# Optimization experiments

Measured on AMD Instinct MI355X. Metric: run time of the kernel, lower is better.

The kernel has to match this reference:

```python
import jax, jax.numpy as jnp
import numpy as np

B, N, F_IN, D, DEPTH = 16, 1024, 80, 64, 4
BN_EPS = 1e-5

def setup_inputs() -> dict:
    key = jax.random.key(0)
    ks = jax.random.split(key, 24)
    def xavier(k, shape, gain):
        fan_in, fan_out = shape[0], shape[-1]
        a = gain * np.sqrt(6.0 / (fan_in + fan_out))
        return jax.random.uniform(k, shape, jnp.float32, -a, a)
    g_relu = float(np.sqrt(2.0))
    g_lrelu = float(np.sqrt(2.0 / (1 + 0.01 ** 2)))
    adj = jax.random.randint(ks[0], (B, N, N), 0, 2, jnp.int32)
    X = jax.random.normal(ks[1], (B, N, F_IN), jnp.float32)
    root_list = jax.random.randint(ks[2], (B, DEPTH, N), 0, 2).astype(jnp.float32)
    W0 = xavier(ks[3], (F_IN, D), g_lrelu)
    Wl = jnp.stack([xavier(ks[4 + i], (D, D), g_relu) for i in range(3)])
    a1l = jnp.stack([xavier(ks[7 + i], (D, 1), g_relu)[:, 0] for i in range(3)])
    a2l = jnp.stack([xavier(ks[10 + i], (D, 1), g_relu)[:, 0] for i in range(3)])
    P = xavier(ks[13], (1, D), g_relu)
    def linear(k, din, dout):
        a = 1.0 / np.sqrt(din)
        k1, k2 = jax.random.split(k)
        return (jax.random.uniform(k1, (din, dout), jnp.float32, -a, a),
                jax.random.uniform(k2, (dout,), jnp.float32, -a, a))
    pW1, pb1 = linear(ks[14], D, 128)
    pW2, pb2 = linear(ks[15], 128, 64)
    pW3, pb3 = linear(ks[16], 64, 2)
    bn = lambda n: (jnp.ones((n,), jnp.float32), jnp.zeros((n,), jnp.float32),
                    jnp.zeros((n,), jnp.float32), jnp.ones((n,), jnp.float32))
    g1, be1, m1, v1 = bn(128)
    g2, be2, m2, v2 = bn(64)
    return dict(adj=adj, X=X, root_list=root_list, W0=W0, Wl=Wl, a1l=a1l, a2l=a2l, P=P,
                pW1=pW1, pb1=pb1, g1=g1, be1=be1, m1=m1, v1=v1,
                pW2=pW2, pb2=pb2, g2=g2, be2=be2, m2=m2, v2=v2,
                pW3=pW3, pb3=pb3)

def reference(adj, X, root_list, W0, Wl, a1l, a2l, P,
              pW1, pb1, g1, be1, m1, v1, pW2, pb2, g2, be2, m2, v2, pW3, pb3):
    relu = jax.nn.relu
    # initial feature change
    h = relu(jnp.einsum('bnf,fd->bnd', X, W0))
    adj_pos = adj > 0
    for i in range(DEPTH - 1):
        root = root_list[:, DEPTH - 1 - i, :]            # [B,N]
        h0 = h
        hW = relu(jnp.einsum('bnd,de->bne', h, Wl[i]))    # [B,N,D]
        t1 = jnp.einsum('bnd,d->bn', hW, a1l[i])
        t2 = jnp.einsum('bnd,d->bn', hW, a2l[i])
        e = relu(t1[:, :, None] + t2[:, None, :])         # [B,N,N]
        # NOTE: original uses -9e15 * zeros_like(adj) == 0 as the masked fill value
        e = jnp.where(adj_pos, e, jnp.zeros((), e.dtype))
        att = jax.nn.softmax(e, axis=-1)
        emb = jnp.einsum('bnm,bmd->bnd', att, hW)
        # assign = root^T @ ones broadcasts root over d
        h = jnp.where(root[:, :, None] > 0, emb, h0)
    # readout attention over root nodes (last root used: depth index 1)
    root = root_list[:, 1, :]
    e = relu(jnp.einsum('d,bnd->bn', P[0], h))
    e = jnp.where(root > 0, e, jnp.float32(-9e15))
    att = jax.nn.softmax(e, axis=-1)
    out = jnp.einsum('bn,bnd->bd', att, h)                # [B,D]
    # prediction head (eval mode: BN uses running stats, dropout off)
    def bn_apply(x, g, be, m, v):
        return (x - m) * jax.lax.rsqrt(v + BN_EPS) * g + be
    x = relu(bn_apply(out @ pW1 + pb1, g1, be1, m1, v1))
    x = relu(bn_apply(x @ pW2 + pb2, g2, be2, m2, v2))
    logits = relu(x @ pW3 + pb3)
    return jax.nn.softmax(logits, axis=-1)
```

## Files before the change

kernel.cpp:

```cpp
#include <hip/hip_runtime.h>
#include <hip/hip_bf16.h>
#include <math.h>

#define B 16
#define N 1024
#define F_IN 80
#define D 64
#define DEPTH 4
#define BN_EPS 1e-5f

typedef __attribute__((ext_vector_type(8))) short  short8v;
typedef __attribute__((ext_vector_type(4))) float  float4v;

union AFrag { unsigned int u[4]; short8v s; };

__device__ __forceinline__ unsigned short f2bf_rne(float x) {
    unsigned int u = __float_as_uint(x);
    unsigned int r = u + 0x7FFFu + ((u >> 16) & 1u);
    return (unsigned short)(r >> 16);
}
__device__ __forceinline__ float bf2f(unsigned short b) {
    return __uint_as_float(((unsigned int)b) << 16);
}

__global__ __launch_bounds__(256) void k_pack(const int* __restrict__ adj,
                                              unsigned short* __restrict__ packS) {
    int gid = blockIdx.x * 256 + threadIdx.x;
    const int4* ap = (const int4*)adj + (size_t)gid * 4;
    unsigned int m = 0;
#pragma unroll
    for (int i = 0; i < 4; ++i) {
        int4 v = ap[i];
        m |= (unsigned int)(v.x > 0) << (i * 4 + 0);
        m |= (unsigned int)(v.y > 0) << (i * 4 + 1);
        m |= (unsigned int)(v.z > 0) << (i * 4 + 2);
        m |= (unsigned int)(v.w > 0) << (i * 4 + 3);
    }
    packS[gid] = (unsigned short)m;
}

__global__ __launch_bounds__(256) void k_h0(const float* __restrict__ X,
                                            const float* __restrict__ W0,
                                            float* __restrict__ h) {
    int b = blockIdx.x >> 6, n0 = (blockIdx.x & 63) << 4;
    int t = threadIdx.x;
    __shared__ float w0s[F_IN * D];
    __shared__ float xs[16 * F_IN];
    for (int j = t; j < F_IN * D; j += 256) w0s[j] = W0[j];
    const float* xp = X + ((size_t)(b * N + n0)) * F_IN;
    for (int j = t; j < 16 * F_IN; j += 256) xs[j] = xp[j];
    __syncthreads();
    int d = t & 63, wid = t >> 6;
    float acc[4] = {0.f, 0.f, 0.f, 0.f};
    for (int f = 0; f < F_IN; ++f) {
        float wv = w0s[f * D + d];
#pragma unroll
        for (int j = 0; j < 4; ++j) acc[j] += xs[(wid * 4 + j) * F_IN + f] * wv;
    }
    float* hp = h + ((size_t)(b * N + n0 + wid * 4)) * D + d;
#pragma unroll
    for (int j = 0; j < 4; ++j) hp[(size_t)j * D] = fmaxf(acc[j], 0.f);
}

__global__ __launch_bounds__(256) void k_hw(const float* __restrict__ h,
                                            const float* __restrict__ Wl,
                                            const float* __restrict__ a1,
                                            const float* __restrict__ a2,
                                            unsigned short* __restrict__ hWhi,
                                            unsigned short* __restrict__ hWlo,
                                            float* __restrict__ t1,
                                            float* __restrict__ t2) {
    int b = blockIdx.x >> 6, n0 = (blockIdx.x & 63) << 4;
    int t = threadIdx.x;
    __shared__ float wls[D * D];
    __shared__ float hs[16 * D];
    for (int j = t; j < D * D; j += 256) wls[j] = Wl[j];
    const float* hp = h + ((size_t)(b * N + n0)) * D;
    for (int j = t; j < 16 * D; j += 256) hs[j] = hp[j];
    __syncthreads();
    int d = t & 63, wid = t >> 6;
    float acc[4] = {0.f, 0.f, 0.f, 0.f};
    for (int k = 0; k < D; ++k) {
        float wv = wls[k * D + d];
#pragma unroll
        for (int j = 0; j < 4; ++j) acc[j] += hs[(wid * 4 + j) * D + k] * wv;
    }
    float a1d = a1[d], a2d = a2[d];
    unsigned short* Hb = hWhi + (size_t)b * (N * D);
    unsigned short* Lb = hWlo + (size_t)b * (N * D);
#pragma unroll
    for (int j = 0; j < 4; ++j) {
        int m = n0 + wid * 4 + j;
        float v = fmaxf(acc[j], 0.f);
        unsigned short vh = f2bf_rne(v);
        unsigned short vl = f2bf_rne(v - bf2f(vh));
        int kb = m >> 5, i = m & 7;
        int lb = ((m >> 3) & 3) * 16 + (d & 15), dt = d >> 4;
        int off = ((kb * 4 + dt) * 64 + lb) * 8 + i;
        Hb[off] = vh; Lb[off] = vl;
        float p1 = v * a1d, p2 = v * a2d;
#pragma unroll
        for (int o = 32; o > 0; o >>= 1) {
            p1 += __shfl_down(p1, o);
            p2 += __shfl_down(p2, o);
        }
        if (d == 0) { t1[b * N + m] = p1; t2[b * N + m] = p2; }
    }
}

__global__ __launch_bounds__(256, 4) void k_att(
    const unsigned short* __restrict__ hWhi, const unsigned short* __restrict__ hWlo,
    const float* __restrict__ t1, const float* __restrict__ t2,
    const unsigned long long* __restrict__ packA,
    const float* __restrict__ root_list, int ridx, float* __restrict__ h)
{
    int vb = (blockIdx.x & 7) * 128 + (blockIdx.x >> 3);
    int b  = vb >> 6;
    int n0 = (vb & 63) << 4;
    int t = threadIdx.x, lane = t & 63, wid = t >> 6;

    __shared__ float t2s[N];
    __shared__ float redsum[4][16];
    __shared__ float invs[16];
    __shared__ float4v part[4][4][64];

    ((float4v*)t2s)[t] = ((const float4v*)(t2 + b * N))[t];
    __syncthreads();

    int r  = lane & 15;
    int qg = wid * 4 + (lane >> 4);
    int n  = n0 + r;
    float t1v = t1[b * N + n];
    const unsigned long long* prow = packA + ((size_t)(b * N + n)) * 16;
    const short8v* BH = (const short8v*)(hWhi + (size_t)b * (N * D));
    const short8v* BL = (const short8v*)(hWlo + (size_t)b * (N * D));

    float4v acc0 = {0,0,0,0}, acc1 = {0,0,0,0}, acc2 = {0,0,0,0}, acc3 = {0,0,0,0};
    float lsum = 0.f;

#pragma unroll
    for (int p = 0; p < 8; ++p) {
        int kb = p * 4 + wid;
        int bi = (kb * 4) * 64 + lane;
        short8v bh0 = BH[bi], bh1 = BH[bi + 64], bh2 = BH[bi + 128], bh3 = BH[bi + 192];
        short8v bl0 = BL[bi], bl1 = BL[bi + 64], bl2 = BL[bi + 128], bl3 = BL[bi + 192];

        unsigned long long word = prow[p * 2 + (qg >> 3)];
        unsigned int mbyte = (unsigned int)(word >> ((qg & 7) * 8)) & 0xFFu;

        const float* t2p = t2s + p * 128 + qg * 8;
        float4v ta = ((const float4v*)t2p)[0];
        float4v tb = ((const float4v*)t2p)[1];

        float wv[8];
#pragma unroll
        for (int i = 0; i < 8; ++i) {
            float t2v = (i < 4) ? ta[i & 3] : tb[i & 3];
            float e = ((mbyte >> i) & 1u) ? fmaxf(t1v + t2v, 0.f) : 0.f;
            float w = __expf(e);
            wv[i] = w;
            lsum += w;
        }

        AFrag fh, fl;
#pragma unroll
        for (int i = 0; i < 4; ++i) {
            unsigned short h0 = f2bf_rne(wv[2 * i]);
            unsigned short h1 = f2bf_rne(wv[2 * i + 1]);
            unsigned short l0 = f2bf_rne(wv[2 * i] - bf2f(h0));
            unsigned short l1 = f2bf_rne(wv[2 * i + 1] - bf2f(h1));
            fh.u[i] = (unsigned int)h0 | ((unsigned int)h1 << 16);
            fl.u[i] = (unsigned int)l0 | ((unsigned int)l1 << 16);
        }

        acc0 = __builtin_amdgcn_mfma_f32_16x16x32_bf16(fh.s, bh0, acc0, 0, 0, 0);
        acc0 = __builtin_amdgcn_mfma_f32_16x16x32_bf16(fh.s, bl0, acc0, 0, 0, 0);
        acc0 = __builtin_amdgcn_mfma_f32_16x16x32_bf16(fl.s, bh0, acc0, 0, 0, 0);
        acc1 = __builtin_amdgcn_mfma_f32_16x16x32_bf16(fh.s, bh1, acc1, 0, 0, 0);
        acc1 = __builtin_amdgcn_mfma_f32_16x16x32_bf16(fh.s, bl1, acc1, 0, 0, 0);
        acc1 = __builtin_amdgcn_mfma_f32_16x16x32_bf16(fl.s, bh1, acc1, 0, 0, 0);
        acc2 = __builtin_amdgcn_mfma_f32_16x16x32_bf16(fh.s, bh2, acc2, 0, 0, 0);
        acc2 = __builtin_amdgcn_mfma_f32_16x16x32_bf16(fh.s, bl2, acc2, 0, 0, 0);
        acc2 = __builtin_amdgcn_mfma_f32_16x16x32_bf16(fl.s, bh2, acc2, 0, 0, 0);
        acc3 = __builtin_amdgcn_mfma_f32_16x16x32_bf16(fh.s, bh3, acc3, 0, 0, 0);
        acc3 = __builtin_amdgcn_mfma_f32_16x16x32_bf16(fh.s, bl3, acc3, 0, 0, 0);
        acc3 = __builtin_amdgcn_mfma_f32_16x16x32_bf16(fl.s, bh3, acc3, 0, 0, 0);
    }

    lsum += __shfl_xor(lsum, 16);
    lsum += __shfl_xor(lsum, 32);
    if (lane < 16) redsum[wid][lane] = lsum;

    part[wid][0][lane] = acc0;
    part[wid][1][lane] = acc1;
    part[wid][2][lane] = acc2;
    part[wid][3][lane] = acc3;
    __syncthreads();
    if (t < 16) invs[t] = 1.0f / (redsum[0][t] + redsum[1][t] + redsum[2][t] + redsum[3][t]);
    __syncthreads();

    int c = t & 63, rg = t >> 6;
    int ls = rg * 16 + (c & 15), dt = c >> 4;
    float4v s = part[0][dt][ls] + part[1][dt][ls] + part[2][dt][ls] + part[3][dt][ls];
    const float* rl = root_list + ((size_t)b * DEPTH + ridx) * N;
#pragma unroll
    for (int reg = 0; reg < 4; ++reg) {
        int rr = rg * 4 + reg;
        if (rl[n0 + rr] > 0.f)
            h[((size_t)(b * N + n0 + rr)) * D + c] = s[reg] * invs[rr];
    }
}

__global__ __launch_bounds__(256) void k_dotw(const float* __restrict__ h,
                                              const float* __restrict__ root_list,
                                              const float* __restrict__ P,
                                              float* __restrict__ wg) {
    int b = blockIdx.x >> 4, n0 = (blockIdx.x & 15) << 6;
    int t = threadIdx.x;
    int r = n0 + (t >> 2), sub = t & 3;
    const float4* hp = (const float4*)(h + ((size_t)(b * N + r)) * D + sub * 16);
    const float4* pp = (const float4*)(P + sub * 16);
    float s = 0.f;
#pragma unroll
    for (int i = 0; i < 4; ++i) {
        float4 hv = hp[i], pv = pp[i];
        s += hv.x * pv.x + hv.y * pv.y + hv.z * pv.z + hv.w * pv.w;
    }
    s += __shfl_xor(s, 1);
    s += __shfl_xor(s, 2);
    if (sub == 0) {
        float rv = root_list[((size_t)b * DEPTH + 1) * N + r];
        wg[b * N + r] = (rv > 0.f) ? fmaxf(s, 0.f) : -9e15f;
    }
}

__global__ __launch_bounds__(1024) void k_pool2(const float* __restrict__ h,
                       const float* __restrict__ wg,
                       const float* __restrict__ pW1, const float* __restrict__ pb1,
                       const float* __restrict__ g1, const float* __restrict__ be1,
                       const float* __restrict__ m1, const float* __restrict__ v1,
                       const float* __restrict__ pW2, const float* __restrict__ pb2,
                       const float* __restrict__ g2, const float* __restrict__ be2,
                       const float* __restrict__ m2, const float* __restrict__ v2,
                       const float* __restrict__ pW3, const float* __restrict__ pb3,
                       float* __restrict__ out) {
    int b = blockIdx.x, t = threadIdx.x, lane = t & 63, wid = t >> 6;
    __shared__ float ws[N];
    __shared__ float red[16];
    __shared__ float part[16][D];
    __shared__ float od[D];
    __shared__ float x1[128];
    __shared__ float x2[64];
    __shared__ float lg[2];

    const float* hb = h + (size_t)b * N * D;
    float sc = wg[b * N + t];

    float lmax = sc;
#pragma unroll
    for (int o = 32; o > 0; o >>= 1) lmax = fmaxf(lmax, __shfl_xor(lmax, o));
    if (lane == 0) red[wid] = lmax;
    __syncthreads();
    float bmax = red[0];
#pragma unroll
    for (int k = 1; k < 16; ++k) bmax = fmaxf(bmax, red[k]);
    __syncthreads();

    float e = __expf(sc - bmax);
    ws[t] = e;
    float lsumv = e;
#pragma unroll
    for (int o = 32; o > 0; o >>= 1) lsumv += __shfl_xor(lsumv, o);
    if (lane == 0) red[wid] = lsumv;
    __syncthreads();
    float bsum = 0.f;
#pragma unroll
    for (int k = 0; k < 16; ++k) bsum += red[k];
    float inv = 1.0f / bsum;

    float acc = 0.f;
    for (int n = wid * 64; n < wid * 64 + 64; ++n) acc += ws[n] * hb[(size_t)n * D + lane];
    part[wid][lane] = acc;
    __syncthreads();
    if (t < D) {
        float s = 0.f;
#pragma unroll
        for (int k = 0; k < 16; ++k) s += part[k][t];
        od[t] = s * inv;
    }
    __syncthreads();

    if (t < 128) {
        float s = pb1[t];
#pragma unroll
        for (int k = 0; k < D; ++k) s += od[k] * pW1[k * 128 + t];
        s = (s - m1[t]) * rsqrtf(v1[t] + BN_EPS) * g1[t] + be1[t];
        x1[t] = fmaxf(s, 0.f);
    }
    __syncthreads();
    if (t < 64) {
        float s = pb2[t];
#pragma unroll
        for (int k = 0; k < 128; ++k) s += x1[k] * pW2[k * 64 + t];
        s = (s - m2[t]) * rsqrtf(v2[t] + BN_EPS) * g2[t] + be2[t];
        x2[t] = fmaxf(s, 0.f);
    }
    __syncthreads();
    if (t < 2) {
        float s = pb3[t];
#pragma unroll
        for (int k = 0; k < 64; ++k) s += x2[k] * pW3[k * 2 + t];
        lg[t] = fmaxf(s, 0.f);
    }
    __syncthreads();
    if (t < 2) {
        float mm = fmaxf(lg[0], lg[1]);
        float e0 = __expf(lg[0] - mm), e1 = __expf(lg[1] - mm);
        out[b * 2 + t] = ((t == 0) ? e0 : e1) / (e0 + e1);
    }
}

extern "C" void kernel_launch(void* const* d_in, const int* in_sizes, int n_in,
                              void* d_out, int out_size, void* d_ws, size_t ws_size,
                              hipStream_t stream) {
    const int*   adj = (const int*)d_in[0];
    const float* X   = (const float*)d_in[1];
    const float* rl  = (const float*)d_in[2];
    const float* W0  = (const float*)d_in[3];
    const float* Wl  = (const float*)d_in[4];
    const float* a1l = (const float*)d_in[5];
    const float* a2l = (const float*)d_in[6];
    const float* P   = (const float*)d_in[7];
    const float* pW1 = (const float*)d_in[8];
    const float* pb1 = (const float*)d_in[9];
    const float* g1  = (const float*)d_in[10];
    const float* be1 = (const float*)d_in[11];
    const float* m1  = (const float*)d_in[12];
    const float* v1  = (const float*)d_in[13];
    const float* pW2 = (const float*)d_in[14];
    const float* pb2 = (const float*)d_in[15];
    const float* g2  = (const float*)d_in[16];
    const float* be2 = (const float*)d_in[17];
    const float* m2  = (const float*)d_in[18];
    const float* v2  = (const float*)d_in[19];
    const float* pW3 = (const float*)d_in[20];
    const float* pb3 = (const float*)d_in[21];
    float* out = (float*)d_out;

    float*          h    = (float*)d_ws;
    unsigned short* hWhi = (unsigned short*)(h + (size_t)B * N * D);
    unsigned short* hWlo = hWhi + (size_t)B * N * D;
    float*          t1   = (float*)(hWlo + (size_t)B * N * D);
    float*          t2   = t1 + B * N;
    unsigned long long* packA = (unsigned long long*)(t2 + B * N);
    float*          wg   = t1;

    k_pack<<<B * N * N / 16 / 256, 256, 0, stream>>>(adj, (unsigned short*)packA);
    k_h0<<<B * 64, 256, 0, stream>>>(X, W0, h);
    for (int i = 0; i < DEPTH - 1; ++i) {
        k_hw<<<B * 64, 256, 0, stream>>>(h, Wl + i * D * D, a1l + i * D, a2l + i * D,
                                         hWhi, hWlo, t1, t2);
        k_att<<<B * 64, 256, 0, stream>>>(hWhi, hWlo, t1, t2, packA, rl,
                                          DEPTH - 1 - i, h);
    }
    k_dotw<<<B * 16, 256, 0, stream>>>(h, rl, P, wg);
    k_pool2<<<B, 1024, 0, stream>>>(h, wg, pW1, pb1, g1, be1, m1, v1,
                                    pW2, pb2, g2, be2, m2, v2, pW3, pb3, out);
}
```

Baseline: 267.2 us.

## Vectorize shared loads, pack hW stores, cheapen bf16 split, partially unroll att loop

The k_h0 and k_hw kernels now stage weights and activations into shared memory with float4 loads. k_hw packs the four bf16 hi/lo values per thread into single uint2 stores instead of scalar 16-bit stores. In k_att the attention-weight hi/lo split now truncates with bit masks instead of round-to-nearest, which cuts ALU work but slightly changes the residual split. The main loop is unrolled by two instead of fully, which may lower register pressure at the cost of some scheduling freedom.

```diff
diff --git a/kernel.cpp b/kernel.cpp
--- a/kernel.cpp
+++ b/kernel.cpp
@@ -21,6 +21,15 @@
 }
 __device__ __forceinline__ float bf2f(unsigned short b) {
     return __uint_as_float(((unsigned int)b) << 16);
+}
+__device__ __forceinline__ void split_pair(float w0, float w1,
+                                           unsigned int& hi, unsigned int& lo) {
+    unsigned int u0 = __float_as_uint(w0), u1 = __float_as_uint(w1);
+    unsigned int h0 = u0 & 0xFFFF0000u,   h1 = u1 & 0xFFFF0000u;
+    hi = (h0 >> 16) | h1;
+    float r0 = w0 - __uint_as_float(h0);
+    float r1 = w1 - __uint_as_float(h1);
+    lo = (__float_as_uint(r0) >> 16) | (__float_as_uint(r1) & 0xFFFF0000u);
 }
 
 __global__ __launch_bounds__(256) void k_pack(const int* __restrict__ adj,
@@ -46,9 +55,11 @@
     int t = threadIdx.x;
     __shared__ float w0s[F_IN * D];
     __shared__ float xs[16 * F_IN];
-    for (int j = t; j < F_IN * D; j += 256) w0s[j] = W0[j];
+    for (int j = t; j < F_IN * D / 4; j += 256)
+        ((float4*)w0s)[j] = ((const float4*)W0)[j];
     const float* xp = X + ((size_t)(b * N + n0)) * F_IN;
-    for (int j = t; j < 16 * F_IN; j += 256) xs[j] = xp[j];
+    for (int j = t; j < 16 * F_IN / 4; j += 256)
+        ((float4*)xs)[j] = ((const float4*)xp)[j];
     __syncthreads();
     int d = t & 63, wid = t >> 6;
     float acc[4] = {0.f, 0.f, 0.f, 0.f};
@@ -74,9 +85,10 @@
     int t = threadIdx.x;
     __shared__ float wls[D * D];
     __shared__ float hs[16 * D];
-    for (int j = t; j < D * D; j += 256) wls[j] = Wl[j];
+    for (int j = t; j < D * D / 4; j += 256)
+        ((float4*)wls)[j] = ((const float4*)Wl)[j];
     const float* hp = h + ((size_t)(b * N + n0)) * D;
-    for (int j = t; j < 16 * D; j += 256) hs[j] = hp[j];
+    if (t < 16 * D / 4) ((float4*)hs)[t] = ((const float4*)hp)[t];
     __syncthreads();
     int d = t & 63, wid = t >> 6;
     float acc[4] = {0.f, 0.f, 0.f, 0.f};
@@ -86,25 +98,37 @@
         for (int j = 0; j < 4; ++j) acc[j] += hs[(wid * 4 + j) * D + k] * wv;
     }
     float a1d = a1[d], a2d = a2[d];
-    unsigned short* Hb = hWhi + (size_t)b * (N * D);
-    unsigned short* Lb = hWlo + (size_t)b * (N * D);
+
+    float v[4];
+    unsigned short vh[4], vl[4];
 #pragma unroll
     for (int j = 0; j < 4; ++j) {
-        int m = n0 + wid * 4 + j;
-        float v = fmaxf(acc[j], 0.f);
-        unsigned short vh = f2bf_rne(v);
-        unsigned short vl = f2bf_rne(v - bf2f(vh));
-        int kb = m >> 5, i = m & 7;
-        int lb = ((m >> 3) & 3) * 16 + (d & 15), dt = d >> 4;
-        int off = ((kb * 4 + dt) * 64 + lb) * 8 + i;
-        Hb[off] = vh; Lb[off] = vl;
-        float p1 = v * a1d, p2 = v * a2d;
+        v[j] = fmaxf(acc[j], 0.f);
+        vh[j] = f2bf_rne(v[j]);
+        vl[j] = f2bf_rne(v[j] - bf2f(vh[j]));
+    }
+    {
+        int m0 = n0 + wid * 4;
+        int kb = m0 >> 5, i0 = m0 & 7;
+        int lb = ((m0 >> 3) & 3) * 16 + (d & 15), dt = d >> 4;
+        size_t off = ((size_t)b * (N * D)) + ((kb * 4 + dt) * 64 + lb) * 8 + i0;
+        uint2 hpack, lpack;
+        hpack.x = (unsigned int)vh[0] | ((unsigned int)vh[1] << 16);
+        hpack.y = (unsigned int)vh[2] | ((unsigned int)vh[3] << 16);
+        lpack.x = (unsigned int)vl[0] | ((unsigned int)vl[1] << 16);
+        lpack.y = (unsigned int)vl[2] | ((unsigned int)vl[3] << 16);
+        *(uint2*)(hWhi + off) = hpack;
+        *(uint2*)(hWlo + off) = lpack;
+    }
+#pragma unroll
+    for (int j = 0; j < 4; ++j) {
+        float p1 = v[j] * a1d, p2 = v[j] * a2d;
 #pragma unroll
         for (int o = 32; o > 0; o >>= 1) {
             p1 += __shfl_down(p1, o);
             p2 += __shfl_down(p2, o);
         }
-        if (d == 0) { t1[b * N + m] = p1; t2[b * N + m] = p2; }
+        if (d == 0) { t1[b * N + n0 + wid * 4 + j] = p1; t2[b * N + n0 + wid * 4 + j] = p2; }
     }
 }
 
@@ -138,7 +162,7 @@
     float4v acc0 = {0,0,0,0}, acc1 = {0,0,0,0}, acc2 = {0,0,0,0}, acc3 = {0,0,0,0};
     float lsum = 0.f;
 
-#pragma unroll
+#pragma unroll 2
     for (int p = 0; p < 8; ++p) {
         int kb = p * 4 + wid;
         int bi = (kb * 4) * 64 + lane;
@@ -164,14 +188,8 @@
 
         AFrag fh, fl;
 #pragma unroll
-        for (int i = 0; i < 4; ++i) {
-            unsigned short h0 = f2bf_rne(wv[2 * i]);
-            unsigned short h1 = f2bf_rne(wv[2 * i + 1]);
-            unsigned short l0 = f2bf_rne(wv[2 * i] - bf2f(h0));
-            unsigned short l1 = f2bf_rne(wv[2 * i + 1] - bf2f(h1));
-            fh.u[i] = (unsigned int)h0 | ((unsigned int)h1 << 16);
-            fl.u[i] = (unsigned int)l0 | ((unsigned int)l1 << 16);
-        }
+        for (int i = 0; i < 4; ++i)
+            split_pair(wv[2 * i], wv[2 * i + 1], fh.u[i], fl.u[i]);
 
         acc0 = __builtin_amdgcn_mfma_f32_16x16x32_bf16(fh.s, bh0, acc0, 0, 0, 0);
         acc0 = __builtin_amdgcn_mfma_f32_16x16x32_bf16(fh.s, bl0, acc0, 0, 0, 0);
```

Measured after the change: 226.8 us. 15.1% less time.
